# Kernel optimization log

Measured on AMD Instinct MI355X. Metric: run time of the kernel, lower is better.

The kernel has to match this reference:

```python
import jax, jax.numpy as jnp
import numpy as np

# Wrapped Conv2D config (channels_last): input 32x32x32 -> output 32x32x64, 3x3 'same', stride 1
H, W, C_IN, C_OUT = 32, 32, 32, 64


def _propagate(w, b, kernel, bias):
    # w: [B, H*W*C_OUT, n_out], b: [B, n_out]
    B, _, n_out = w.shape
    # transpose(0,2,1) + reshape to [B, n_out, H, W, C_OUT]
    wt = jnp.transpose(w, (0, 2, 1)).reshape(B, n_out, H, W, C_OUT)
    # bias-sum reduction: sum over (h, w, c) of w * bias[c], added to b
    b_new = jnp.einsum('bnhwc,c->bn', wt, bias) + b
    # Batched transposed conv over all n_out slices at once (replaces K.rnn loop)
    z = wt.reshape(B * n_out, H, W, C_OUT)
    w_in = jax.lax.conv_transpose(
        z, kernel, strides=(1, 1), padding='SAME',
        dimension_numbers=('NHWC', 'HWIO', 'NHWC'), transpose_kernel=True)
    # -> [B*n_out, H, W, C_IN]; flatten and transpose back to [B, n_in, n_out]
    w_new = jnp.transpose(w_in.reshape(B, n_out, H * W * C_IN), (0, 2, 1))
    return w_new, b_new


def setup_inputs() -> dict:
    key = jax.random.key(0)
    ks = jax.random.split(key, 6)
    B, n_out = 8, 32
    n_flat = H * W * C_OUT
    return {
        'w_out_u': jax.random.normal(ks[0], (B, n_flat, n_out), jnp.float32),
        'b_out_u': jax.random.normal(ks[1], (B, n_out), jnp.float32),
        'w_out_l': jax.random.normal(ks[2], (B, n_flat, n_out), jnp.float32),
        'b_out_l': jax.random.normal(ks[3], (B, n_out), jnp.float32),
        'kernel': jax.random.normal(ks[4], (3, 3, C_IN, C_OUT), jnp.float32) * 0.1,
        'bias': jax.random.normal(ks[5], (C_OUT,), jnp.float32) * 0.1,
    }


def reference(w_out_u, b_out_u, w_out_l, b_out_l, kernel, bias):
    w_u, b_u = _propagate(w_out_u, b_out_u, kernel, bias)
    w_l, b_l = _propagate(w_out_l, b_out_l, kernel, bias)
    return (w_u, b_u, w_l, b_l)
```

## Files before the change

### kernel.cpp

```cpp
#include <hip/hip_runtime.h>
#include <hip/hip_bf16.h>

#define H  32
#define W  32
#define CI 32
#define CO 64
#define NB 8
#define NOUT 32

#define WU_OFF 0
#define BU_OFF (NB * H * W * CI * NOUT)
#define WL_OFF (BU_OFF + NB * NOUT)
#define BL_OFF (WL_OFF + NB * H * W * CI * NOUT)

#define KF_UINT4 2304
#define BP_OFF_BYTES 36864

typedef __bf16 bf16x8 __attribute__((ext_vector_type(8)));
typedef float  f32x4  __attribute__((ext_vector_type(4)));

__device__ __forceinline__ unsigned int pack_bf16(float lo, float hi) {
    unsigned int ulo = __float_as_uint(lo) + 0x8000u;
    unsigned int uhi = __float_as_uint(hi) + 0x8000u;
    return (uhi & 0xffff0000u) | (ulo >> 16);
}

__global__ void prep_kernel(const float* __restrict__ K,
                            unsigned int* __restrict__ kws,
                            float* __restrict__ bp) {
    int bx = blockIdx.x, t = threadIdx.x;
    if (bx < 9) {
        int g    = bx * 256 + t;
        int tap  = g >> 8;
        int r    = g & 255;
        int i    = r >> 3;
        int og   = r & 7;
        int c    = og >> 2;
        int quad = og & 3;
        int ih   = i >> 4;
        int lane = quad * 16 + (i & 15);
        int dst  = ((tap * 4 + c * 2 + ih) * 64 + lane) * 4;
        const float4* src = (const float4*)(K + (size_t)g * 8);
        float4 f0 = src[0];
        float4 f1 = src[1];
        kws[dst + 0] = pack_bf16(f0.x, f0.y);
        kws[dst + 1] = pack_bf16(f0.z, f0.w);
        kws[dst + 2] = pack_bf16(f1.x, f1.y);
        kws[dst + 3] = pack_bf16(f1.z, f1.w);
    } else {
        bp[(bx - 9) * 256 + t] = 0.f;
    }
}

__global__ __launch_bounds__(512, 2)
void fused_conv_kernel(const float* __restrict__ in0,
                       const float* __restrict__ in1,
                       const uint4* __restrict__ kws,
                       const float* __restrict__ bias,
                       float* __restrict__ bp,
                       float* __restrict__ out0,
                       float* __restrict__ out1) {
    __shared__ uint4 kf[KF_UINT4];
    __shared__ uint4 stg[3 * 18 * 4 * 32];
    __shared__ float bias_s[CO];

    int t = threadIdx.x;
    for (int k = t; k < KF_UINT4; k += 512) kf[k] = kws[k];
    if (t < CO) bias_s[t] = bias[t];

    int bx    = blockIdx.x;
    int x     = bx & 7;
    int q     = bx >> 3;
    int combo = x * 2 + (q >> 6);
    int idx   = q & 63;
    int side  = combo >> 3;
    int b     = combo & 7;
    int h     = idx >> 1;
    int wh    = idx & 1;

    const float* inp = (side ? in1 : in0) + (size_t)b * 1024 * 2048;

    int unit = t >> 5;
    int ogp  = (t >> 3) & 3;
    int n4   = t & 7;
    int wave = t >> 6;
    int lane = t & 63;
    int n16  = lane & 15;
    int quad = lane >> 4;

    f32x4 acc[2][2][2] = {};
    float sb[4] = {0.f, 0.f, 0.f, 0.f};
    const bf16x8* kfp = (const bf16x8*)kf;

    for (int c = 0; c < 2; c++) {
        __syncthreads();
        for (int s = 0; s < 4; s++) {
            int tile = s * 16 + unit;
            if (tile >= 54) break;
            int row = tile / 18;
            int col = tile - row * 18;
            int hi  = h - 1 + row;
            int wi  = wh * 16 - 1 + col;
            if (hi < 0 || hi >= H || wi < 0 || wi >= W) continue;
            const float* p = inp + (size_t)(hi * W + wi) * 2048
                           + c * 1024 + ogp * 256 + n4 * 4;
            float v[8][4];
#pragma unroll
            for (int j = 0; j < 8; j++) {
                float4 f = *(const float4*)(p + j * 32);
                v[j][0] = f.x; v[j][1] = f.y; v[j][2] = f.z; v[j][3] = f.w;
            }
            if (row == 1 && col >= 1 && col <= 16) {
#pragma unroll
                for (int j = 0; j < 8; j++) {
                    float bj = bias_s[c * 32 + ogp * 8 + j];
#pragma unroll
                    for (int k = 0; k < 4; k++)
                        sb[k] = fmaf(v[j][k], bj, sb[k]);
                }
            }
            uint4* dst = &stg[tile * 128 + ogp * 32];
#pragma unroll
            for (int k = 0; k < 4; k++) {
                uint4 u;
                u.x = pack_bf16(v[0][k], v[1][k]);
                u.y = pack_bf16(v[2][k], v[3][k]);
                u.z = pack_bf16(v[4][k], v[5][k]);
                u.w = pack_bf16(v[6][k], v[7][k]);
                dst[(n4 * 4 + k) ^ ogp] = u;
            }
        }
        __syncthreads();
#pragma unroll
        for (int p2 = 0; p2 < 2; p2++) {
            int wl = wave * 2 + p2;
            int w  = wh * 16 + wl;
#pragma unroll
            for (int kh = 0; kh < 3; kh++) {
                int hi = h + 1 - kh;
                if (hi < 0 || hi >= H) continue;
                int row = 2 - kh;
#pragma unroll
                for (int kw = 0; kw < 3; kw++) {
                    int wi = w + 1 - kw;
                    if (wi < 0 || wi >= W) continue;
                    int col = wl + 2 - kw;
                    int tap = kh * 3 + kw;
                    const uint4* Tp = &stg[(row * 18 + col) * 128];
                    union { uint4 u; bf16x8 v; } b0, b1;
                    b0.u = Tp[quad * 32 + (n16 ^ quad)];
                    b1.u = Tp[quad * 32 + (n16 ^ quad) + 16];
                    bf16x8 a0 = kfp[(tap * 4 + c * 2 + 0) * 64 + lane];
                    bf16x8 a1 = kfp[(tap * 4 + c * 2 + 1) * 64 + lane];
                    acc[p2][0][0] = __builtin_amdgcn_mfma_f32_16x16x32_bf16(a0, b0.v, acc[p2][0][0], 0, 0, 0);
                    acc[p2][0][1] = __builtin_amdgcn_mfma_f32_16x16x32_bf16(a0, b1.v, acc[p2][0][1], 0, 0, 0);
                    acc[p2][1][0] = __builtin_amdgcn_mfma_f32_16x16x32_bf16(a1, b0.v, acc[p2][1][0], 0, 0, 0);
                    acc[p2][1][1] = __builtin_amdgcn_mfma_f32_16x16x32_bf16(a1, b1.v, acc[p2][1][1], 0, 0, 0);
                }
            }
        }
    }

#pragma unroll
    for (int off = 8; off <= 32; off <<= 1)
#pragma unroll
        for (int k = 0; k < 4; k++)
            sb[k] += __shfl_xor(sb[k], off, 64);
    if (lane < 8) {
#pragma unroll
        for (int k = 0; k < 4; k++)
            atomicAdd(&bp[side * 256 + b * 32 + n4 * 4 + k], sb[k]);
    }

    float* outp = (side ? out1 : out0) + (size_t)b * (H * W * CI * NOUT);
#pragma unroll
    for (int p2 = 0; p2 < 2; p2++) {
        int w = wh * 16 + wave * 2 + p2;
        float* wout = outp + (size_t)((h * W + w) * CI) * NOUT;
#pragma unroll
        for (int ih = 0; ih < 2; ih++)
#pragma unroll
            for (int nh = 0; nh < 2; nh++)
#pragma unroll
                for (int r = 0; r < 4; r++) {
                    int i = ih * 16 + quad * 4 + r;
                    int n = nh * 16 + n16;
                    wout[i * NOUT + n] = acc[p2][ih][nh][r];
                }
    }
}

__global__ void bias_final32_kernel(const float* __restrict__ bp,
                                    const float* __restrict__ bu,
                                    const float* __restrict__ bl,
                                    float* __restrict__ out) {
    int sb = blockIdx.x;
    int t  = threadIdx.x;
    if (t >= NOUT) return;
    int side = sb >> 3, b = sb & 7;
    const float* bb = side ? bl : bu;
    out[(side ? BL_OFF : BU_OFF) + b * NOUT + t] =
        bb[b * NOUT + t] + bp[sb * 32 + t];
}

extern "C" void kernel_launch(void* const* d_in, const int* in_sizes, int n_in,
                              void* d_out, int out_size, void* d_ws, size_t ws_size,
                              hipStream_t stream) {
    const float* wu   = (const float*)d_in[0];
    const float* bu   = (const float*)d_in[1];
    const float* wl   = (const float*)d_in[2];
    const float* bl   = (const float*)d_in[3];
    const float* K    = (const float*)d_in[4];
    const float* bias = (const float*)d_in[5];
    float* out = (float*)d_out;
    unsigned int* kws = (unsigned int*)d_ws;
    float* bp = (float*)((char*)d_ws + BP_OFF_BYTES);

    prep_kernel<<<dim3(11), dim3(256), 0, stream>>>(K, kws, bp);
    fused_conv_kernel<<<dim3(1024), dim3(512), 0, stream>>>(
        wu, wl, (const uint4*)d_ws, bias, bp, out + WU_OFF, out + WL_OFF);
    bias_final32_kernel<<<dim3(16), dim3(64), 0, stream>>>(bp, bu, bl, out);
}
```

Measured before the change: 228.7 us.

## Halve conv tile width, load weights to registers, new LDS swizzle, raise MFMA priority

Each block now covers 8 output columns with 256 threads instead of 16 columns with 512, and the grid doubles to 2048 blocks. The bf16 weight fragments are no longer copied into shared memory; each wave loads them straight from global memory into registers once per channel chunk, which cuts LDS use. The staging swizzle adds an extra XOR term to reduce LDS bank conflicts, and setprio raises wave priority around the MFMA loop. In exchange, halo rows are re-read more often (10/8 columns instead of 18/16), and 18 register-held weight vectors add register pressure.

```diff
diff --git a/kernel.cpp b/kernel.cpp
--- a/kernel.cpp
+++ b/kernel.cpp
@@ -52,7 +52,7 @@
     }
 }
 
-__global__ __launch_bounds__(512, 2)
+__global__ __launch_bounds__(256, 2)
 void fused_conv_kernel(const float* __restrict__ in0,
                        const float* __restrict__ in1,
                        const uint4* __restrict__ kws,
@@ -60,25 +60,24 @@
                        float* __restrict__ bp,
                        float* __restrict__ out0,
                        float* __restrict__ out1) {
-    __shared__ uint4 kf[KF_UINT4];
-    __shared__ uint4 stg[3 * 18 * 4 * 32];
+    __shared__ uint4 stg[30 * 128];
     __shared__ float bias_s[CO];
 
     int t = threadIdx.x;
-    for (int k = t; k < KF_UINT4; k += 512) kf[k] = kws[k];
     if (t < CO) bias_s[t] = bias[t];
 
     int bx    = blockIdx.x;
     int x     = bx & 7;
     int q     = bx >> 3;
-    int combo = x * 2 + (q >> 6);
-    int idx   = q & 63;
+    int combo = x * 2 + (q >> 7);
+    int idx   = q & 127;
     int side  = combo >> 3;
     int b     = combo & 7;
-    int h     = idx >> 1;
-    int wh    = idx & 1;
+    int h     = idx >> 2;
+    int wq    = idx & 3;
 
     const float* inp = (side ? in1 : in0) + (size_t)b * 1024 * 2048;
+    const bf16x8* kfp = (const bf16x8*)kws;
 
     int unit = t >> 5;
     int ogp  = (t >> 3) & 3;
@@ -90,51 +89,62 @@
 
     f32x4 acc[2][2][2] = {};
     float sb[4] = {0.f, 0.f, 0.f, 0.f};
-    const bf16x8* kfp = (const bf16x8*)kf;
+    int rbase = quad * 32 + ((n16 ^ (n16 >> 2)) ^ quad);
+
+    __syncthreads();
 
     for (int c = 0; c < 2; c++) {
-        __syncthreads();
+        bf16x8 a[9][2];
+#pragma unroll
+        for (int tap = 0; tap < 9; tap++) {
+            a[tap][0] = kfp[(tap * 4 + c * 2 + 0) * 64 + lane];
+            a[tap][1] = kfp[(tap * 4 + c * 2 + 1) * 64 + lane];
+        }
         for (int s = 0; s < 4; s++) {
-            int tile = s * 16 + unit;
-            if (tile >= 54) break;
-            int row = tile / 18;
-            int col = tile - row * 18;
-            int hi  = h - 1 + row;
-            int wi  = wh * 16 - 1 + col;
-            if (hi < 0 || hi >= H || wi < 0 || wi >= W) continue;
-            const float* p = inp + (size_t)(hi * W + wi) * 2048
-                           + c * 1024 + ogp * 256 + n4 * 4;
-            float v[8][4];
-#pragma unroll
-            for (int j = 0; j < 8; j++) {
-                float4 f = *(const float4*)(p + j * 32);
-                v[j][0] = f.x; v[j][1] = f.y; v[j][2] = f.z; v[j][3] = f.w;
-            }
-            if (row == 1 && col >= 1 && col <= 16) {
-#pragma unroll
-                for (int j = 0; j < 8; j++) {
-                    float bj = bias_s[c * 32 + ogp * 8 + j];
-#pragma unroll
-                    for (int k = 0; k < 4; k++)
-                        sb[k] = fmaf(v[j][k], bj, sb[k]);
+            int tile = s * 8 + unit;
+            if (tile < 30) {
+                int row = tile >= 20 ? 2 : (tile >= 10 ? 1 : 0);
+                int col = tile - row * 10;
+                int hi  = h - 1 + row;
+                int wi  = wq * 8 - 1 + col;
+                if (hi >= 0 && hi < H && wi >= 0 && wi < W) {
+                    const float* p = inp + (size_t)(hi * W + wi) * 2048
+                                   + c * 1024 + ogp * 256 + n4 * 4;
+                    float v[8][4];
+#pragma unroll
+                    for (int j = 0; j < 8; j++) {
+                        float4 f = *(const float4*)(p + j * 32);
+                        v[j][0] = f.x; v[j][1] = f.y; v[j][2] = f.z; v[j][3] = f.w;
+                    }
+                    if (row == 1 && col >= 1 && col <= 8) {
+#pragma unroll
+                        for (int j = 0; j < 8; j++) {
+                            float bj = bias_s[c * 32 + ogp * 8 + j];
+#pragma unroll
+                            for (int k = 0; k < 4; k++)
+                                sb[k] = fmaf(v[j][k], bj, sb[k]);
+                        }
+                    }
+                    uint4* dst = &stg[tile * 128 + ogp * 32];
+#pragma unroll
+                    for (int k = 0; k < 4; k++) {
+                        uint4 u;
+                        u.x = pack_bf16(v[0][k], v[1][k]);
+                        u.y = pack_bf16(v[2][k], v[3][k]);
+                        u.z = pack_bf16(v[4][k], v[5][k]);
+                        u.w = pack_bf16(v[6][k], v[7][k]);
+                        int n = n4 * 4 + k;
+                        dst[(n ^ (n >> 2)) ^ ogp] = u;
+                    }
                 }
-            }
-            uint4* dst = &stg[tile * 128 + ogp * 32];
-#pragma unroll
-            for (int k = 0; k < 4; k++) {
-                uint4 u;
-                u.x = pack_bf16(v[0][k], v[1][k]);
-                u.y = pack_bf16(v[2][k], v[3][k]);
-                u.z = pack_bf16(v[4][k], v[5][k]);
-                u.w = pack_bf16(v[6][k], v[7][k]);
-                dst[(n4 * 4 + k) ^ ogp] = u;
             }
         }
         __syncthreads();
+        __builtin_amdgcn_s_setprio(1);
 #pragma unroll
         for (int p2 = 0; p2 < 2; p2++) {
             int wl = wave * 2 + p2;
-            int w  = wh * 16 + wl;
+            int w  = wq * 8 + wl;
 #pragma unroll
             for (int kh = 0; kh < 3; kh++) {
                 int hi = h + 1 - kh;
@@ -146,19 +156,19 @@
                     if (wi < 0 || wi >= W) continue;
                     int col = wl + 2 - kw;
                     int tap = kh * 3 + kw;
-                    const uint4* Tp = &stg[(row * 18 + col) * 128];
+                    const uint4* Tp = &stg[(row * 10 + col) * 128];
                     union { uint4 u; bf16x8 v; } b0, b1;
-                    b0.u = Tp[quad * 32 + (n16 ^ quad)];
-                    b1.u = Tp[quad * 32 + (n16 ^ quad) + 16];
-                    bf16x8 a0 = kfp[(tap * 4 + c * 2 + 0) * 64 + lane];
-                    bf16x8 a1 = kfp[(tap * 4 + c * 2 + 1) * 64 + lane];
-                    acc[p2][0][0] = __builtin_amdgcn_mfma_f32_16x16x32_bf16(a0, b0.v, acc[p2][0][0], 0, 0, 0);
-                    acc[p2][0][1] = __builtin_amdgcn_mfma_f32_16x16x32_bf16(a0, b1.v, acc[p2][0][1], 0, 0, 0);
-                    acc[p2][1][0] = __builtin_amdgcn_mfma_f32_16x16x32_bf16(a1, b0.v, acc[p2][1][0], 0, 0, 0);
-                    acc[p2][1][1] = __builtin_amdgcn_mfma_f32_16x16x32_bf16(a1, b1.v, acc[p2][1][1], 0, 0, 0);
+                    b0.u = Tp[rbase];
+                    b1.u = Tp[rbase ^ 20];
+                    acc[p2][0][0] = __builtin_amdgcn_mfma_f32_16x16x32_bf16(a[tap][0], b0.v, acc[p2][0][0], 0, 0, 0);
+                    acc[p2][0][1] = __builtin_amdgcn_mfma_f32_16x16x32_bf16(a[tap][0], b1.v, acc[p2][0][1], 0, 0, 0);
+                    acc[p2][1][0] = __builtin_amdgcn_mfma_f32_16x16x32_bf16(a[tap][1], b0.v, acc[p2][1][0], 0, 0, 0);
+                    acc[p2][1][1] = __builtin_amdgcn_mfma_f32_16x16x32_bf16(a[tap][1], b1.v, acc[p2][1][1], 0, 0, 0);
                 }
             }
         }
+        __builtin_amdgcn_s_setprio(0);
+        if (c == 0) __syncthreads();
     }
 
 #pragma unroll
@@ -175,7 +185,7 @@
     float* outp = (side ? out1 : out0) + (size_t)b * (H * W * CI * NOUT);
 #pragma unroll
     for (int p2 = 0; p2 < 2; p2++) {
-        int w = wh * 16 + wave * 2 + p2;
+        int w = wq * 8 + wave * 2 + p2;
         float* wout = outp + (size_t)((h * W + w) * CI) * NOUT;
 #pragma unroll
         for (int ih = 0; ih < 2; ih++)
@@ -217,7 +227,7 @@
     float* bp = (float*)((char*)d_ws + BP_OFF_BYTES);
 
     prep_kernel<<<dim3(11), dim3(256), 0, stream>>>(K, kws, bp);
-    fused_conv_kernel<<<dim3(1024), dim3(512), 0, stream>>>(
+    fused_conv_kernel<<<dim3(2048), dim3(256), 0, stream>>>(
         wu, wl, (const uint4*)d_ws, bias, bp, out + WU_OFF, out + WL_OFF);
     bias_final32_kernel<<<dim3(16), dim3(64), 0, stream>>>(bp, bu, bl, out);
 }
```

Result: faster. 219.8 us (-3.9%).
